# Kernel optimization log

Hardware: AMD Instinct MI355X
Metric: run time of the kernel (lower is better)

The kernel has to match this reference:

```python
import jax, jax.numpy as jnp
import numpy as np

B, N, D = 8, 2048, 768
LN_EPS = 1e-5


def setup_inputs() -> dict:
    key = jax.random.key(0)
    ks = jax.random.split(key, 5)
    scale = 1.0 / np.sqrt(D)
    features = jax.random.normal(ks[0], (B, N, D), dtype=jnp.float32)
    mask = jax.random.randint(ks[1], (B, N), 0, 2) == 1  # True = masked (padding)
    Wq = jax.random.normal(ks[2], (D, D), dtype=jnp.float32) * scale
    Wk = jax.random.normal(ks[3], (D, D), dtype=jnp.float32) * scale
    Wv = jax.random.normal(ks[4], (D, D), dtype=jnp.float32) * scale
    ln_gamma = jnp.ones((D,), dtype=jnp.float32)
    ln_beta = jnp.zeros((D,), dtype=jnp.float32)
    return {"features": features, "mask": mask, "Wq": Wq, "Wk": Wk, "Wv": Wv,
            "ln_gamma": ln_gamma, "ln_beta": ln_beta}


def reference(features, mask, Wq, Wk, Wv, ln_gamma, ln_beta):
    # LayerNorm over last dim
    mu = jnp.mean(features, axis=-1, keepdims=True)
    var = jnp.mean(jnp.square(features - mu), axis=-1, keepdims=True)
    x = (features - mu) * jax.lax.rsqrt(var + LN_EPS) * ln_gamma + ln_beta
    # torch Linear: y = x @ W.T
    Q = jnp.einsum('bnd,ed->bne', x, Wq)
    K = jnp.einsum('bnd,ed->bne', x, Wk)
    V = jnp.einsum('bnd,ed->bne', x, Wv)
    scale = x.shape[-1] ** -0.5
    scores = jnp.einsum('bnd,bmd->bnm', Q, K) * scale  # [B,N,N]
    scores = jnp.where(mask[:, None, :], -jnp.inf, scores)
    probs = jax.nn.softmax(scores, axis=-1)
    ctx = jnp.einsum('bnm,bmd->bnd', probs, V)
    return ctx
```

## Files before the change

### kernel.cpp

```cpp
#include <hip/hip_runtime.h>
#include <hip/hip_bf16.h>
#include <cstdint>

typedef __attribute__((ext_vector_type(8))) __bf16 bf16v8;
typedef __attribute__((ext_vector_type(4))) float f32x4;
typedef __attribute__((ext_vector_type(4))) unsigned short ushort4v;
typedef __attribute__((ext_vector_type(8))) unsigned short ushort8v;

#define BB 8
#define NN 2048
#define DD 768

__device__ __forceinline__ float b2f(unsigned short u) {
  union { unsigned int i; float f; } c; c.i = ((unsigned int)u) << 16; return c.f;
}
__device__ __forceinline__ unsigned short f2b(float f) {
  union { float f; unsigned int i; } c; c.f = f;
  unsigned int u = c.i;
  return (unsigned short)((u + 0x7fffu + ((u >> 16) & 1u)) >> 16);
}

__global__ __launch_bounds__(256) void prep(
    const float* __restrict__ x, const float* __restrict__ gamma, const float* __restrict__ beta,
    unsigned short* __restrict__ xb,
    const float* __restrict__ Wq, const float* __restrict__ Wk, const float* __restrict__ Wv,
    unsigned short* __restrict__ Wcat,
    const int* __restrict__ mask, int* __restrict__ kidx, int* __restrict__ ncnt) {
  __shared__ float red[2][4];
  __shared__ int wsum[4];
  const int bid = blockIdx.x;
  const int t = threadIdx.x;

  if (bid < BB * NN) {
    const int row = bid;
    const float* xr = x + (size_t)row * DD;
    float a0 = xr[t], a1 = xr[t + 256], a2 = xr[t + 512];
    float s = a0 + a1 + a2;
    float q = a0 * a0 + a1 * a1 + a2 * a2;
    for (int o = 32; o > 0; o >>= 1) { s += __shfl_xor(s, o); q += __shfl_xor(q, o); }
    int w = t >> 6, lane = t & 63;
    if (lane == 0) { red[0][w] = s; red[1][w] = q; }
    __syncthreads();
    s = red[0][0] + red[0][1] + red[0][2] + red[0][3];
    q = red[1][0] + red[1][1] + red[1][2] + red[1][3];
    float mean = s * (1.0f / DD);
    float var = q * (1.0f / DD) - mean * mean;
    float inv = rsqrtf(var + 1e-5f);
    unsigned short* o0 = xb + (size_t)row * DD;
    o0[t]       = f2b((a0 - mean) * inv * gamma[t]       + beta[t]);
    o0[t + 256] = f2b((a1 - mean) * inv * gamma[t + 256] + beta[t + 256]);
    o0[t + 512] = f2b((a2 - mean) * inv * gamma[t + 512] + beta[t + 512]);
  } else if (bid < BB * NN + 6912) {
    const int i = (bid - BB * NN) * 256 + t;
    const int dd = DD * DD;
    if (i < 3 * dd) {
      float v;
      if (i < dd)           v = Wq[i] * 0.03608439182435161f;
      else if (i < 2 * dd)  v = Wk[i - dd];
      else                  v = Wv[i - 2 * dd];
      Wcat[i] = f2b(v);
    }
  } else {
    const int b = bid - (BB * NN + 6912);
    const int* mr = mask + b * NN;
#pragma unroll
    for (int j = 0; j < 8; ++j) kidx[b * NN + t * 8 + j] = 0;
    int v[8]; int s = 0;
#pragma unroll
    for (int j = 0; j < 8; ++j) { v[j] = (mr[t * 8 + j] == 0) ? 1 : 0; s += v[j]; }
    int lane = t & 63, w = t >> 6;
    int xp = s;
    for (int o = 1; o < 64; o <<= 1) { int y = __shfl_up(xp, o); if (lane >= o) xp += y; }
    if (lane == 63) wsum[w] = xp;
    __syncthreads();
    int base = 0;
#pragma unroll
    for (int i = 0; i < 4; ++i) if (i < w) base += wsum[i];
    int run = base + xp - s;
#pragma unroll
    for (int j = 0; j < 8; ++j) { if (v[j]) kidx[b * NN + run] = t * 8 + j; run += v[j]; }
    if (t == 255) ncnt[b] = base + xp;
  }
}

__global__ __launch_bounds__(256) void xc_gather(const unsigned short* __restrict__ Xb,
                                                 const int* __restrict__ kidx,
                                                 const int* __restrict__ ncnt,
                                                 unsigned short* __restrict__ Xc) {
  const int b = blockIdx.y;
  const int nc = ncnt[b];
  const int r256 = (nc + 255) & ~255;
  const int row0 = blockIdx.x * 16;
  if (row0 >= r256) return;
  int off = 0;
#pragma unroll
  for (int i = 0; i < 8; ++i) if (i < b) off += (ncnt[i] + 255) & ~255;
  for (int u = threadIdx.x; u < 16 * 96; u += 256) {
    const int r = row0 + u / 96;
    const int ch = (u % 96) * 8;
    if (r >= r256) continue;
    ushort8v val = {0, 0, 0, 0, 0, 0, 0, 0};
    if (r < nc)
      val = *(const ushort8v*)&Xb[((size_t)b * NN + kidx[b * NN + r]) * DD + ch];
    *(ushort8v*)&Xc[(size_t)(off + r) * DD + ch] = val;
  }
}

__device__ __forceinline__ void gload_lds16(const void* g, void* l) {
  __builtin_amdgcn_global_load_lds(
      (const __attribute__((address_space(1))) void*)g,
      (__attribute__((address_space(3))) void*)(unsigned)(uintptr_t)l,
      16, 0, 0);
}

#define RDA(i0, ks, B)                                                                   \
  _Pragma("unroll")                                                                      \
  for (int i_ = 0; i_ < 4; ++i_)                                                         \
    aq[i_] = *(const bf16v8*)&smem[(B) + (ks) * 8192 + arow0 + ((i0) + i_) * 512 + kg8];
#define RDB(ks, B)                                                                       \
  _Pragma("unroll")                                                                      \
  for (int j_ = 0; j_ < NJ; ++j_)                                                        \
    bq[j_] = *(const bf16v8*)&smem[(B) + 16384 + (ks) * 8192 + brow0 + j_ * 512 + kg8];
#define MFQ(i0)                                                                          \
  _Pragma("unroll")                                                                      \
  for (int i_ = 0; i_ < 4; ++i_) {                                                       \
    _Pragma("unroll")                                                                    \
    for (int j_ = 0; j_ < NJ; ++j_)                                                      \
      acc[(i0) + i_][j_] = __builtin_amdgcn_mfma_f32_16x16x32_bf16(                      \
          aq[i_], bq[j_], acc[(i0) + i_][j_], 0, 0, 0);                                  \
  }
#define BARF asm volatile("s_barrier" ::: "memory")
#define VMC6 asm volatile("s_waitcnt vmcnt(6)" ::: "memory")
#define VMC3 asm volatile("s_waitcnt vmcnt(3)" ::: "memory")
#define VMC0 asm volatile("s_waitcnt vmcnt(0)" ::: "memory")
#define P1   __builtin_amdgcn_s_setprio(1)
#define P0   __builtin_amdgcn_s_setprio(0)

#define TILEK(KT, CURB, NXTB)                                                            \
  do {                                                                                   \
    RDA(0, 0, CURB); RDB(0, CURB);                                                       \
    if ((KT) + 1 < NT) stgA((KT) + 1, 1, (NXTB));                                        \
    BARF; P1; MFQ(0); P0; BARF;                                                          \
    RDA(4, 0, CURB);                                                                     \
    if ((KT) + 1 < NT) stgB((KT) + 1, 1, (NXTB));                                        \
    BARF; P1; MFQ(4); P0;                                                                \
    VMC6; BARF;                                                                          \
    RDA(0, 1, CURB); RDB(1, CURB);                                                       \
    if ((KT) + 2 < NT) stgA((KT) + 2, 0, (CURB));                                        \
    BARF; P1; MFQ(0); P0; BARF;                                                          \
    RDA(4, 1, CURB);                                                                     \
    if ((KT) + 2 < NT) stgB((KT) + 2, 0, (CURB));                                        \
    BARF; P1; MFQ(4); P0;                                                                \
    if ((KT) < NT - 2) { VMC6; } else { VMC0; }                                          \
    BARF;                                                                                \
  } while (0)

template <int NJ>
__global__ __launch_bounds__(512, 2) void gemmCtx(
    const unsigned short* __restrict__ A, const unsigned short* __restrict__ Bm,
    float* __restrict__ Cf, int lda, int ldb,
    long aStride, long bStride, long cStride,
    const int* __restrict__ ncnt) {
  extern __shared__ unsigned short smem[];
  const int BN = NJ * 64;

  const int t = threadIdx.x;
  int bx = blockIdx.x, by = blockIdx.y, bz = blockIdx.z;
  {
    const int gx = gridDim.x, gy = gridDim.y;
    const int nwg = gx * gy * (int)gridDim.z;
    int id = bx + gx * (by + gy * bz);
    int sw = (id & 7) * (nwg >> 3) + (id >> 3);
    bx = sw % gx; int r2 = sw / gx;
    by = r2 % gy; bz = r2 / gy;
  }
  const int n0 = bx * BN, m0 = by * 256;
  const int NT = ((ncnt[bz] + 127) >> 7) << 1;

  const unsigned short* Ab = A + (size_t)bz * aStride;
  const unsigned short* Bb = Bm + (size_t)bz * bStride;

  const int lane = t & 63;
  const int w = t >> 6;
  const int wm = w >> 2, wn = w & 3;
  const int frow = lane & 15;
  const int kg8 = (lane >> 4) * 8;
  const int arow0 = (wm * 128 + frow) * 32;
  const int brow0 = (wn * (NJ * 16) + frow) * 32;

  const int srow = t >> 2;
  const int scol8 = (t & 3) * 8;
  const unsigned short* Asrc = Ab + (size_t)(m0 + srow) * lda + scol8;
  const unsigned short* Bsrc = Bb + (size_t)(n0 + srow) * ldb + scol8;
  const int sdst = w * 512;

  auto stgA = [&](int kt, int ks, int bufb) {
    const unsigned short* s = Asrc + kt * 64 + ks * 32;
    gload_lds16(s, &smem[bufb + ks * 8192 + sdst]);
    gload_lds16(s + (size_t)128 * lda, &smem[bufb + ks * 8192 + 4096 + sdst]);
  };
  auto stgB = [&](int kt, int ks, int bufb) {
    const unsigned short* s = Bsrc + kt * 64 + ks * 32;
    gload_lds16(s, &smem[bufb + 16384 + ks * 8192 + sdst]);
    gload_lds16(s + (size_t)128 * ldb, &smem[bufb + 16384 + ks * 8192 + 4096 + sdst]);
  };

  f32x4 acc[8][NJ] = {};
  bf16v8 aq[4], bq[NJ];

  stgA(0, 0, 0);     stgB(0, 0, 0);
  stgA(0, 1, 0);     stgB(0, 1, 0);
  stgA(1, 0, 32768); stgB(1, 0, 32768);
  asm volatile("s_waitcnt vmcnt(8)" ::: "memory");
  BARF;

  for (int ktp = 0; ktp < NT; ktp += 2) {
    TILEK(ktp, 0, 32768);
    TILEK(ktp + 1, 32768, 0);
  }

  const int r0 = (lane >> 4) * 4;
  const int c0 = lane & 15;
  const int mrowB = m0 + wm * 128 + r0;
  const int ncolB = n0 + wn * (NJ * 16) + c0;
  float* dst = Cf + (size_t)bz * cStride;
#pragma unroll
  for (int i = 0; i < 8; ++i)
#pragma unroll
    for (int j = 0; j < NJ; ++j)
#pragma unroll
      for (int r = 0; r < 4; ++r)
        dst[(size_t)(mrowB + i * 16 + r) * DD + (ncolB + j * 16)] = acc[i][j][r];
}

template <int NJ>
__global__ __launch_bounds__(512, 2) void gemmQKV(
    const unsigned short* __restrict__ Xb, const unsigned short* __restrict__ Xc,
    const unsigned short* __restrict__ Wcat,
    unsigned short* __restrict__ Qb, unsigned short* __restrict__ Kc,
    unsigned short* __restrict__ Vtc, const int* __restrict__ ncnt) {
  extern __shared__ unsigned short smem[];
  constexpr int NT = 12;

  const int t = threadIdx.x;
  const int bid = (int)blockIdx.x;
  const int lid = (bid & 7) * 64 + (bid >> 3);

  const int lane = t & 63;
  const int w = t >> 6;
  const int wm = w >> 2, wn = w & 3;
  const int frow = lane & 15;
  const int kg8 = (lane >> 4) * 8;
  const int arow0 = (wm * 128 + frow) * 32;
  const int brow0 = (wn * (NJ * 16) + frow) * 32;
  const int srow = t >> 2;
  const int scol8 = (t & 3) * 8;
  const int sdst = w * 512;

  const bool isQ = lid < 192;
  const unsigned short* Asrc;
  const unsigned short* Bsrc;
  int m0 = 0, ncolQ = 0, b = 0, cbase0 = 0, ni = 0;
  if (isQ) {
    m0 = (lid / 3) * 256;
    ncolQ = (lid % 3) * 256;
    Asrc = Xb + (size_t)(m0 + srow) * DD + scol8;
    Bsrc = Wcat + (size_t)(ncolQ + srow) * DD + scol8;
  } else {
    int offv[9]; offv[0] = 0;
#pragma unroll
    for (int i = 0; i < 8; ++i) offv[i + 1] = offv[i] + ((ncnt[i] + 255) & ~255);
    const int GT = offv[8] >> 8;
    const int kid = lid - 192;
    if (kid >= GT * 6) return;
    const int gt = kid / 6; ni = kid % 6;
#pragma unroll
    for (int i = 1; i < 8; ++i) if (offv[i] <= gt * 256) b = i;
    cbase0 = gt * 256 - offv[b];
    Asrc = Xc + (size_t)(gt * 256 + srow) * DD + scol8;
    Bsrc = Wcat + (size_t)(768 + ni * 256 + srow) * DD + scol8;
  }

  auto stgA = [&](int kt, int ks, int bufb) {
    const unsigned short* s = Asrc + kt * 64 + ks * 32;
    gload_lds16(s, &smem[bufb + ks * 8192 + sdst]);
    gload_lds16(s + (size_t)128 * DD, &smem[bufb + ks * 8192 + 4096 + sdst]);
  };
  auto stgB = [&](int kt, int ks, int bufb) {
    const unsigned short* s = Bsrc + kt * 64 + ks * 32;
    gload_lds16(s, &smem[bufb + 16384 + ks * 8192 + sdst]);
    gload_lds16(s + (size_t)128 * DD, &smem[bufb + 16384 + ks * 8192 + 4096 + sdst]);
  };

  f32x4 acc[8][NJ] = {};
  bf16v8 aq[4], bq[NJ];

  stgA(0, 0, 0);     stgB(0, 0, 0);
  stgA(0, 1, 0);     stgB(0, 1, 0);
  stgA(1, 0, 32768); stgB(1, 0, 32768);
  asm volatile("s_waitcnt vmcnt(8)" ::: "memory");
  BARF;

  for (int ktp = 0; ktp < NT; ktp += 2) {
    TILEK(ktp, 0, 32768);
    TILEK(ktp + 1, 32768, 0);
  }

  const int r0 = (lane >> 4) * 4;
  const int c0 = lane & 15;
  if (isQ) {
    const int mrowB = m0 + wm * 128 + r0;
    const int ncolB = ncolQ + wn * (NJ * 16) + c0;
#pragma unroll
    for (int i = 0; i < 8; ++i)
#pragma unroll
      for (int j = 0; j < NJ; ++j)
#pragma unroll
        for (int r = 0; r < 4; ++r)
          Qb[(size_t)(mrowB + i * 16 + r) * DD + (ncolB + j * 16)] = f2b(acc[i][j][r]);
  } else {
    const int rowL = wm * 128 + r0;
    const int ncolL = ni * 256 + wn * (NJ * 16) + c0;
    const int cbase = cbase0 + rowL;
    if (ni < 3) {
      unsigned short* dst = Kc + (size_t)b * NN * DD;
#pragma unroll
      for (int i = 0; i < 8; ++i)
#pragma unroll
        for (int j = 0; j < NJ; ++j)
#pragma unroll
          for (int r = 0; r < 4; ++r)
            dst[(size_t)(cbase + i * 16 + r) * DD + (ncolL + j * 16)] = f2b(acc[i][j][r]);
    } else {
#pragma unroll
      for (int i = 0; i < 8; ++i) {
#pragma unroll
        for (int j = 0; j < NJ; ++j) {
          const int e = ncolL + j * 16 - 768;
          ushort4v pk;
#pragma unroll
          for (int r = 0; r < 4; ++r) pk[r] = f2b(acc[i][j][r]);
          *(ushort4v*)&Vtc[((size_t)b * DD + e) * NN + cbase + i * 16] = pk;
        }
      }
    }
  }
}

__global__ __launch_bounds__(512, 2) void gemm1P(
    const unsigned short* __restrict__ Qa, const unsigned short* __restrict__ Kn,
    unsigned short* __restrict__ So, const int* __restrict__ ncnt) {
  extern __shared__ unsigned short smem[];
  constexpr int NT = 12;

  const int t = threadIdx.x;
  const int lane = t & 63;
  const int w = t >> 6;
  const int wm = w >> 2, wn = w & 3;
  const int frow = lane & 15;
  const int kg8 = (lane >> 4) * 8;
  const int arow0 = (wm * 64 + frow) * 32;
  const int brow0 = (wn * 64 + frow) * 32;
  const int srow = t >> 2;
  const int scol8 = (t & 3) * 8;
  const int sdst = w * 512;
  const int r0 = (lane >> 4) * 4;
  const int c0 = lane & 15;

  int nbv[8];
#pragma unroll
  for (int b_ = 0; b_ < 8; ++b_) nbv[b_] = (ncnt[b_] + 255) >> 8;

  f32x4 acc[4][4];
  bf16v8 aq[4], bq[4];

#pragma unroll 1
  for (int it = 0; it < 4; ++it) {
    int rem = (int)blockIdx.x + it * 256;
    int b = 0;
#pragma unroll 1
    for (; b < 8; ++b) { int c = nbv[b] * 16; if (rem < c) break; rem -= c; }
    if (b >= 8) break;
    const int ni = rem >> 4, mi = rem & 15;
    const int m0 = mi * 128, n0 = ni * 256;

    const unsigned short* Asrc = Qa + ((size_t)b * NN + m0 + srow) * DD + scol8;
    const unsigned short* Bsrc = Kn + ((size_t)b * NN + n0 + srow) * DD + scol8;

    auto stgA = [&](int kt, int ks, int bufb) {
      gload_lds16(Asrc + kt * 64 + ks * 32, &smem[bufb + ks * 4096 + sdst]);
    };
    auto stgB = [&](int kt, int ks, int bufb) {
      const unsigned short* s = Bsrc + kt * 64 + ks * 32;
      gload_lds16(s, &smem[bufb + 8192 + ks * 8192 + sdst]);
      gload_lds16(s + (size_t)128 * DD, &smem[bufb + 8192 + ks * 8192 + 4096 + sdst]);
    };

#pragma unroll
    for (int i = 0; i < 4; ++i)
#pragma unroll
      for (int j = 0; j < 4; ++j) acc[i][j] = f32x4{0.f, 0.f, 0.f, 0.f};

    stgA(0, 0, 0);     stgB(0, 0, 0);
    stgA(0, 1, 0);     stgB(0, 1, 0);
    stgA(1, 0, 24576); stgB(1, 0, 24576);
    VMC3;
    BARF;

#pragma unroll 1
    for (int kt = 0; kt < NT; ++kt) {
      const int cur = (kt & 1) ? 24576 : 0;
      const int nxt = cur ^ 24576;
#pragma unroll
      for (int i_ = 0; i_ < 4; ++i_)
        aq[i_] = *(const bf16v8*)&smem[cur + arow0 + i_ * 512 + kg8];
#pragma unroll
      for (int j_ = 0; j_ < 4; ++j_)
        bq[j_] = *(const bf16v8*)&smem[cur + 8192 + brow0 + j_ * 512 + kg8];
      if (kt + 1 < NT) { stgA(kt + 1, 1, nxt); stgB(kt + 1, 1, nxt); }
      BARF; P1;
#pragma unroll
      for (int i_ = 0; i_ < 4; ++i_)
#pragma unroll
        for (int j_ = 0; j_ < 4; ++j_)
          acc[i_][j_] = __builtin_amdgcn_mfma_f32_16x16x32_bf16(aq[i_], bq[j_], acc[i_][j_], 0, 0, 0);
      P0; BARF;
#pragma unroll
      for (int i_ = 0; i_ < 4; ++i_)
        aq[i_] = *(const bf16v8*)&smem[cur + 4096 + arow0 + i_ * 512 + kg8];
#pragma unroll
      for (int j_ = 0; j_ < 4; ++j_)
        bq[j_] = *(const bf16v8*)&smem[cur + 16384 + brow0 + j_ * 512 + kg8];
      if (kt + 2 < NT) { stgA(kt + 2, 0, cur); stgB(kt + 2, 0, cur); }
      BARF; P1;
#pragma unroll
      for (int i_ = 0; i_ < 4; ++i_)
#pragma unroll
        for (int j_ = 0; j_ < 4; ++j_)
          acc[i_][j_] = __builtin_amdgcn_mfma_f32_16x16x32_bf16(aq[i_], bq[j_], acc[i_][j_], 0, 0, 0);
      P0;
      if (kt < NT - 2) { VMC3; } else { VMC0; }
      BARF;
    }

    unsigned short* dst = So + (size_t)b * NN * NN;
    const int mrowB = m0 + wm * 64 + r0;
    const int ncolB = n0 + wn * 64 + c0;
#pragma unroll
    for (int i = 0; i < 4; ++i)
#pragma unroll
      for (int j = 0; j < 4; ++j)
#pragma unroll
        for (int r = 0; r < 4; ++r)
          dst[(size_t)(mrowB + i * 16 + r) * NN + (ncolB + j * 16)] = f2b(acc[i][j][r]);
  }
}

__global__ __launch_bounds__(256) void softmax_c(unsigned short* __restrict__ S,
                                                 const int* __restrict__ ncnt) {
  int row = blockIdx.x;
  int bb = row >> 11;
  const int nc = ncnt[bb];
  const int p128 = (nc + 127) & ~127;
  unsigned short* sr = S + (size_t)row * NN;
  int t = threadIdx.x;
  const int cbase = t * 8;

  float v[8];
  const bool anyload = cbase < nc;
  ushort8v pk;
  if (anyload) pk = *(const ushort8v*)&sr[cbase];
  float mx = -1e30f;
#pragma unroll
  for (int j = 0; j < 8; ++j) {
    v[j] = anyload ? b2f(pk[j]) : 0.f;
    if (cbase + j < nc) mx = fmaxf(mx, v[j]);
  }
  for (int o = 32; o > 0; o >>= 1) mx = fmaxf(mx, __shfl_xor(mx, o));
  __shared__ float redm[4], reds[4];
  int w = t >> 6, lane = t & 63;
  if (lane == 0) redm[w] = mx;
  __syncthreads();
  mx = fmaxf(fmaxf(redm[0], redm[1]), fmaxf(redm[2], redm[3]));

  float e[8];
  float sum = 0.f;
#pragma unroll
  for (int j = 0; j < 8; ++j) {
    e[j] = (cbase + j < nc) ? __expf(v[j] - mx) : 0.f;
    sum += e[j];
  }
  for (int o = 32; o > 0; o >>= 1) sum += __shfl_xor(sum, o);
  if (lane == 0) reds[w] = sum;
  __syncthreads();
  sum = reds[0] + reds[1] + reds[2] + reds[3];
  float inv = 1.0f / sum;

  if (cbase < p128) {
    ushort8v op;
#pragma unroll
    for (int j = 0; j < 8; ++j) op[j] = f2b(e[j] * inv);
    *(ushort8v*)&sr[cbase] = op;
  }
}

extern "C" void kernel_launch(void* const* d_in, const int* in_sizes, int n_in,
                              void* d_out, int out_size, void* d_ws, size_t ws_size,
                              hipStream_t stream) {
  const float* features = (const float*)d_in[0];
  const int* mask       = (const int*)d_in[1];
  const float* Wq       = (const float*)d_in[2];
  const float* Wk       = (const float*)d_in[3];
  const float* Wv       = (const float*)d_in[4];
  const float* gamma    = (const float*)d_in[5];
  const float* beta     = (const float*)d_in[6];
  float* out = (float*)d_out;

  char* ws = (char*)d_ws;
  size_t off = 0;
  auto alloc = [&](size_t bytes) {
    char* p = ws + off;
    off += (bytes + 255) & ~(size_t)255;
    return p;
  };
  unsigned short* Wcat = (unsigned short*)alloc((size_t)(2304 + 64) * DD * 2);
  unsigned short* Qb   = (unsigned short*)alloc((size_t)BB * NN * DD * 2);
  unsigned short* Kc   = (unsigned short*)alloc((size_t)BB * NN * DD * 2);
  unsigned short* Vtc  = (unsigned short*)alloc(((size_t)BB * DD + 64) * NN * 2);
  int* kidx = (int*)alloc((size_t)BB * NN * 4);
  int* ncnt = (int*)alloc(64 * 4);
  char* last = alloc((size_t)BB * NN * NN * 2);
  unsigned short* Sb = (unsigned short*)last;
  unsigned short* Xb = (unsigned short*)last;
  unsigned short* Xc = (unsigned short*)(last + (size_t)34 * 1024 * 1024);

  (void)hipFuncSetAttribute(reinterpret_cast<const void*>(&gemmQKV<4>),
                            hipFuncAttributeMaxDynamicSharedMemorySize, 131072);
  (void)hipFuncSetAttribute(reinterpret_cast<const void*>(&gemm1P),
                            hipFuncAttributeMaxDynamicSharedMemorySize, 98304);
  (void)hipFuncSetAttribute(reinterpret_cast<const void*>(&gemmCtx<3>),
                            hipFuncAttributeMaxDynamicSharedMemorySize, 131072);

  prep<<<BB * NN + 6912 + BB, 256, 0, stream>>>(
      features, gamma, beta, Xb, Wq, Wk, Wv, Wcat, mask, kidx, ncnt);

  xc_gather<<<dim3(128, BB), 256, 0, stream>>>(Xb, kidx, ncnt, Xc);

  gemmQKV<4><<<512, 512, 131072, stream>>>(Xb, Xc, Wcat, Qb, Kc, Vtc, ncnt);

  gemm1P<<<256, 512, 98304, stream>>>(Qb, Kc, Sb, ncnt);

  softmax_c<<<BB * NN, 256, 0, stream>>>(Sb, ncnt);

  gemmCtx<3><<<dim3(DD / 192, NN / 256, BB), 512, 131072, stream>>>(
      Sb, Vtc, out, NN, NN,
      (long)NN * NN, (long)DD * NN, (long)NN * DD, ncnt);
}
```

Baseline: 199.5 us.

## Fuse key-row gather into QKV GEMM loads and remap score-GEMM tile order

Drops the separate xc_gather kernel. The QKV GEMM now loads the unmasked key/value rows straight from the normalized activations through the kidx index table, which saves a launch and a round trip through a compacted buffer. The GEMM also loops over up to two work items per block so it copes with larger item counts. Separately, gemm1P remaps block IDs so neighbouring blocks take adjacent tiles, aiming at better cache reuse. Padded rows beyond the unmasked count now read whatever kidx holds instead of zeros, which relies on those entries being valid indices.

```diff
diff --git a/kernel.cpp b/kernel.cpp
--- a/kernel.cpp
+++ b/kernel.cpp
@@ -83,29 +83,6 @@
   }
 }
 
-__global__ __launch_bounds__(256) void xc_gather(const unsigned short* __restrict__ Xb,
-                                                 const int* __restrict__ kidx,
-                                                 const int* __restrict__ ncnt,
-                                                 unsigned short* __restrict__ Xc) {
-  const int b = blockIdx.y;
-  const int nc = ncnt[b];
-  const int r256 = (nc + 255) & ~255;
-  const int row0 = blockIdx.x * 16;
-  if (row0 >= r256) return;
-  int off = 0;
-#pragma unroll
-  for (int i = 0; i < 8; ++i) if (i < b) off += (ncnt[i] + 255) & ~255;
-  for (int u = threadIdx.x; u < 16 * 96; u += 256) {
-    const int r = row0 + u / 96;
-    const int ch = (u % 96) * 8;
-    if (r >= r256) continue;
-    ushort8v val = {0, 0, 0, 0, 0, 0, 0, 0};
-    if (r < nc)
-      val = *(const ushort8v*)&Xb[((size_t)b * NN + kidx[b * NN + r]) * DD + ch];
-    *(ushort8v*)&Xc[(size_t)(off + r) * DD + ch] = val;
-  }
-}
-
 __device__ __forceinline__ void gload_lds16(const void* g, void* l) {
   __builtin_amdgcn_global_load_lds(
       (const __attribute__((address_space(1))) void*)g,
@@ -235,10 +212,10 @@
 
 template <int NJ>
 __global__ __launch_bounds__(512, 2) void gemmQKV(
-    const unsigned short* __restrict__ Xb, const unsigned short* __restrict__ Xc,
-    const unsigned short* __restrict__ Wcat,
+    const unsigned short* __restrict__ Xb, const unsigned short* __restrict__ Wcat,
     unsigned short* __restrict__ Qb, unsigned short* __restrict__ Kc,
-    unsigned short* __restrict__ Vtc, const int* __restrict__ ncnt) {
+    unsigned short* __restrict__ Vtc,
+    const int* __restrict__ kidx, const int* __restrict__ ncnt) {
   extern __shared__ unsigned short smem[];
   constexpr int NT = 12;
 
@@ -256,91 +233,102 @@
   const int srow = t >> 2;
   const int scol8 = (t & 3) * 8;
   const int sdst = w * 512;
-
-  const bool isQ = lid < 192;
-  const unsigned short* Asrc;
-  const unsigned short* Bsrc;
-  int m0 = 0, ncolQ = 0, b = 0, cbase0 = 0, ni = 0;
-  if (isQ) {
-    m0 = (lid / 3) * 256;
-    ncolQ = (lid % 3) * 256;
-    Asrc = Xb + (size_t)(m0 + srow) * DD + scol8;
-    Bsrc = Wcat + (size_t)(ncolQ + srow) * DD + scol8;
-  } else {
-    int offv[9]; offv[0] = 0;
-#pragma unroll
-    for (int i = 0; i < 8; ++i) offv[i + 1] = offv[i] + ((ncnt[i] + 255) & ~255);
-    const int GT = offv[8] >> 8;
-    const int kid = lid - 192;
-    if (kid >= GT * 6) return;
-    const int gt = kid / 6; ni = kid % 6;
-#pragma unroll
-    for (int i = 1; i < 8; ++i) if (offv[i] <= gt * 256) b = i;
-    cbase0 = gt * 256 - offv[b];
-    Asrc = Xc + (size_t)(gt * 256 + srow) * DD + scol8;
-    Bsrc = Wcat + (size_t)(768 + ni * 256 + srow) * DD + scol8;
-  }
-
-  auto stgA = [&](int kt, int ks, int bufb) {
-    const unsigned short* s = Asrc + kt * 64 + ks * 32;
-    gload_lds16(s, &smem[bufb + ks * 8192 + sdst]);
-    gload_lds16(s + (size_t)128 * DD, &smem[bufb + ks * 8192 + 4096 + sdst]);
-  };
-  auto stgB = [&](int kt, int ks, int bufb) {
-    const unsigned short* s = Bsrc + kt * 64 + ks * 32;
-    gload_lds16(s, &smem[bufb + 16384 + ks * 8192 + sdst]);
-    gload_lds16(s + (size_t)128 * DD, &smem[bufb + 16384 + ks * 8192 + 4096 + sdst]);
-  };
-
-  f32x4 acc[8][NJ] = {};
-  bf16v8 aq[4], bq[NJ];
-
-  stgA(0, 0, 0);     stgB(0, 0, 0);
-  stgA(0, 1, 0);     stgB(0, 1, 0);
-  stgA(1, 0, 32768); stgB(1, 0, 32768);
-  asm volatile("s_waitcnt vmcnt(8)" ::: "memory");
-  BARF;
-
-  for (int ktp = 0; ktp < NT; ktp += 2) {
-    TILEK(ktp, 0, 32768);
-    TILEK(ktp + 1, 32768, 0);
-  }
-
   const int r0 = (lane >> 4) * 4;
   const int c0 = lane & 15;
-  if (isQ) {
-    const int mrowB = m0 + wm * 128 + r0;
-    const int ncolB = ncolQ + wn * (NJ * 16) + c0;
+
+  int offv[9]; offv[0] = 0;
+#pragma unroll
+  for (int i = 0; i < 8; ++i) offv[i + 1] = offv[i] + ((ncnt[i] + 255) & ~255);
+  const int GT = offv[8] >> 8;
+  const int nItems = 192 + GT * 6;
+
+  f32x4 acc[8][NJ];
+  bf16v8 aq[4], bq[NJ];
+
+#pragma unroll 1
+  for (int pass = 0; pass < 2; ++pass) {
+    const int item = lid + pass * 512;
+    if (item >= nItems) break;
+    const bool isQ = item < 192;
+    int m0 = 0, ncolQ = 0, b = 0, cbase0 = 0, ni = 0;
+    const unsigned short *Asrc0, *Asrc1, *Bsrc;
+    if (isQ) {
+      m0 = (item / 3) * 256;
+      ncolQ = (item % 3) * 256;
+      Asrc0 = Xb + (size_t)(m0 + srow) * DD + scol8;
+      Asrc1 = Asrc0 + (size_t)128 * DD;
+      Bsrc  = Wcat + (size_t)(ncolQ + srow) * DD + scol8;
+    } else {
+      const int kid = item - 192;
+      const int gt = kid / 6; ni = kid % 6;
+#pragma unroll
+      for (int i = 1; i < 8; ++i) if (offv[i] <= gt * 256) b = i;
+      cbase0 = gt * 256 - offv[b];
+      Asrc0 = Xb + ((size_t)b * NN + kidx[b * NN + cbase0 + srow]) * DD + scol8;
+      Asrc1 = Xb + ((size_t)b * NN + kidx[b * NN + cbase0 + 128 + srow]) * DD + scol8;
+      Bsrc  = Wcat + (size_t)(768 + ni * 256 + srow) * DD + scol8;
+    }
+
+    auto stgA = [&](int kt, int ks, int bufb) {
+      gload_lds16(Asrc0 + kt * 64 + ks * 32, &smem[bufb + ks * 8192 + sdst]);
+      gload_lds16(Asrc1 + kt * 64 + ks * 32, &smem[bufb + ks * 8192 + 4096 + sdst]);
+    };
+    auto stgB = [&](int kt, int ks, int bufb) {
+      const unsigned short* s = Bsrc + kt * 64 + ks * 32;
+      gload_lds16(s, &smem[bufb + 16384 + ks * 8192 + sdst]);
+      gload_lds16(s + (size_t)128 * DD, &smem[bufb + 16384 + ks * 8192 + 4096 + sdst]);
+    };
+
 #pragma unroll
     for (int i = 0; i < 8; ++i)
 #pragma unroll
-      for (int j = 0; j < NJ; ++j)
-#pragma unroll
-        for (int r = 0; r < 4; ++r)
-          Qb[(size_t)(mrowB + i * 16 + r) * DD + (ncolB + j * 16)] = f2b(acc[i][j][r]);
-  } else {
-    const int rowL = wm * 128 + r0;
-    const int ncolL = ni * 256 + wn * (NJ * 16) + c0;
-    const int cbase = cbase0 + rowL;
-    if (ni < 3) {
-      unsigned short* dst = Kc + (size_t)b * NN * DD;
+      for (int j = 0; j < NJ; ++j) acc[i][j] = f32x4{0.f, 0.f, 0.f, 0.f};
+
+    stgA(0, 0, 0);     stgB(0, 0, 0);
+    stgA(0, 1, 0);     stgB(0, 1, 0);
+    stgA(1, 0, 32768); stgB(1, 0, 32768);
+    asm volatile("s_waitcnt vmcnt(8)" ::: "memory");
+    BARF;
+
+    for (int ktp = 0; ktp < NT; ktp += 2) {
+      TILEK(ktp, 0, 32768);
+      TILEK(ktp + 1, 32768, 0);
+    }
+
+    if (isQ) {
+      const int mrowB = m0 + wm * 128 + r0;
+      const int ncolB = ncolQ + wn * (NJ * 16) + c0;
 #pragma unroll
       for (int i = 0; i < 8; ++i)
 #pragma unroll
         for (int j = 0; j < NJ; ++j)
 #pragma unroll
           for (int r = 0; r < 4; ++r)
-            dst[(size_t)(cbase + i * 16 + r) * DD + (ncolL + j * 16)] = f2b(acc[i][j][r]);
+            Qb[(size_t)(mrowB + i * 16 + r) * DD + (ncolB + j * 16)] = f2b(acc[i][j][r]);
     } else {
-#pragma unroll
-      for (int i = 0; i < 8; ++i) {
-#pragma unroll
-        for (int j = 0; j < NJ; ++j) {
-          const int e = ncolL + j * 16 - 768;
-          ushort4v pk;
-#pragma unroll
-          for (int r = 0; r < 4; ++r) pk[r] = f2b(acc[i][j][r]);
-          *(ushort4v*)&Vtc[((size_t)b * DD + e) * NN + cbase + i * 16] = pk;
+      const int rowL = wm * 128 + r0;
+      const int ncolL = ni * 256 + wn * (NJ * 16) + c0;
+      const int cbase = cbase0 + rowL;
+      if (ni < 3) {
+        unsigned short* dst = Kc + (size_t)b * NN * DD;
+#pragma unroll
+        for (int i = 0; i < 8; ++i)
+#pragma unroll
+          for (int j = 0; j < NJ; ++j)
+#pragma unroll
+            for (int r = 0; r < 4; ++r)
+              dst[(size_t)(cbase + i * 16 + r) * DD + (ncolL + j * 16)] = f2b(acc[i][j][r]);
+      } else {
+#pragma unroll
+        for (int i = 0; i < 8; ++i) {
+#pragma unroll
+          for (int j = 0; j < NJ; ++j) {
+            const int e = ncolL + j * 16 - 768;
+            ushort4v pk;
+#pragma unroll
+            for (int r = 0; r < 4; ++r) pk[r] = f2b(acc[i][j][r]);
+            *(ushort4v*)&Vtc[((size_t)b * DD + e) * NN + cbase + i * 16] = pk;
+          }
         }
       }
     }
@@ -354,6 +342,8 @@
   constexpr int NT = 12;
 
   const int t = threadIdx.x;
+  const int bid = (int)blockIdx.x;
+  const int lid = (bid & 7) * 32 + (bid >> 3);
   const int lane = t & 63;
   const int w = t >> 6;
   const int wm = w >> 2, wn = w & 3;
@@ -376,7 +366,7 @@
 
 #pragma unroll 1
   for (int it = 0; it < 4; ++it) {
-    int rem = (int)blockIdx.x + it * 256;
+    int rem = lid * 2 + (it & 1) + (it >> 1) * 512;
     int b = 0;
 #pragma unroll 1
     for (; b < 8; ++b) { int c = nbv[b] * 16; if (rem < c) break; rem -= c; }
@@ -532,7 +522,6 @@
   char* last = alloc((size_t)BB * NN * NN * 2);
   unsigned short* Sb = (unsigned short*)last;
   unsigned short* Xb = (unsigned short*)last;
-  unsigned short* Xc = (unsigned short*)(last + (size_t)34 * 1024 * 1024);
 
   (void)hipFuncSetAttribute(reinterpret_cast<const void*>(&gemmQKV<4>),
                             hipFuncAttributeMaxDynamicSharedMemorySize, 131072);
@@ -544,9 +533,7 @@
   prep<<<BB * NN + 6912 + BB, 256, 0, stream>>>(
       features, gamma, beta, Xb, Wq, Wk, Wv, Wcat, mask, kidx, ncnt);
 
-  xc_gather<<<dim3(128, BB), 256, 0, stream>>>(Xb, kidx, ncnt, Xc);
-
-  gemmQKV<4><<<512, 512, 131072, stream>>>(Xb, Xc, Wcat, Qb, Kc, Vtc, ncnt);
+  gemmQKV<4><<<512, 512, 131072, stream>>>(Xb, Wcat, Qb, Kc, Vtc, kidx, ncnt);
 
   gemm1P<<<256, 512, 98304, stream>>>(Qb, Kc, Sb, ncnt);
 
```

New measurement: 207.6 us. 4.0% more time.
